# Kernel optimization log

Hardware: AMD Instinct MI355X
Metric: run time of the kernel (lower is better)

Reference implementation:

```python
import jax, jax.numpy as jnp
import numpy as np

# tcnn HashGrid config constants
N_LEVELS = 16
F_PER_LEVEL = 2
LOG2_T = 19
T = 1 << LOG2_T          # 524288 entries per level
BASE_RES = 16
PER_LEVEL_SCALE = 2.0
PRIMES = (1, 2654435761)  # tcnn spatial hash primes for 2D

N_POINTS = 4_194_304      # ~2048x2048 pixels


def setup_inputs() -> dict:
    key = jax.random.key(0)
    k1, k2, k3, k4, k5 = jax.random.split(key, 5)
    v_pixel_pos = jax.random.uniform(k1, (N_POINTS, 2), dtype=jnp.float32)
    # tcnn initializes hash grids ~ U(-1e-4, 1e-4); use scaled normals of similar magnitude
    hash_table = jax.random.normal(k2, (N_LEVELS, T, F_PER_LEVEL), dtype=jnp.float32) * 1e-4
    W1 = jax.random.normal(k3, (32, 64), dtype=jnp.float32) * (1.0 / np.sqrt(32).astype(np.float32))
    W2 = jax.random.normal(k4, (64, 64), dtype=jnp.float32) * (1.0 / np.sqrt(64).astype(np.float32))
    W3 = jax.random.normal(k5, (64, 3), dtype=jnp.float32) * (1.0 / np.sqrt(64).astype(np.float32))
    return {"v_pixel_pos": v_pixel_pos, "hash_table": hash_table, "W1": W1, "W2": W2, "W3": W3}


def _hashgrid_encode(pos, table):
    """Multiresolution hash-grid encoding, 2D bilinear. pos: [N,2] in [0,1]; table: [L,T,F]. -> [N, L*F]"""
    feats = []
    for lvl in range(N_LEVELS):  # small fixed loop over levels (structurally distinct resolutions)
        scale = BASE_RES * (PER_LEVEL_SCALE ** lvl) - 1.0
        res = int(np.ceil(scale)) + 1
        p = pos * jnp.float32(scale) + 0.5
        pf = jnp.floor(p)
        w = p - pf                       # bilinear weights, [N,2]
        pi = pf.astype(jnp.uint32)       # base corner, [N,2]
        dense = res * res <= T           # tcnn uses dense indexing when the grid fits
        acc = jnp.zeros((pos.shape[0], F_PER_LEVEL), dtype=table.dtype)
        for dx, dy in ((0, 0), (1, 0), (0, 1), (1, 1)):
            cx = pi[:, 0] + jnp.uint32(dx)
            cy = pi[:, 1] + jnp.uint32(dy)
            if dense:
                idx = cx + cy * jnp.uint32(res)
            else:
                idx = (cx * jnp.uint32(PRIMES[0])) ^ (cy * jnp.uint32(PRIMES[1]))
                idx = idx & jnp.uint32(T - 1)
            wx = w[:, 0] if dx else (1.0 - w[:, 0])
            wy = w[:, 1] if dy else (1.0 - w[:, 1])
            acc = acc + (wx * wy)[:, None] * table[lvl, idx.astype(jnp.int32)]
        feats.append(acc)
    return jnp.concatenate(feats, axis=-1)  # [N, 32]


def reference(v_pixel_pos, hash_table, W1, W2, W3):
    h = _hashgrid_encode(v_pixel_pos, hash_table)   # [N, 32]
    h = jax.nn.relu(h @ W1)                          # [N, 64]
    h = jax.nn.relu(h @ W2)                          # [N, 64]
    return h @ W3                                    # [N, 3], no output activation
```

## Files before the change

### kernel.cpp

```cpp
#include <hip/hip_runtime.h>
#include <hip/hip_fp16.h>


constexpr unsigned TSIZE  = 1u << 19;
constexpr unsigned PRIME2 = 2654435761u;
constexpr int N_HASHED    = 10;
constexpr int LVL0_HASH   = 6;
#define FEAT_SCALE   4096.0f
#define INV_SCALE    (1.0f / 4096.0f)

typedef _Float16 f16x8 __attribute__((ext_vector_type(8)));
typedef float    f32x4 __attribute__((ext_vector_type(4)));
typedef unsigned u32x2 __attribute__((ext_vector_type(2)));
typedef unsigned u32x4 __attribute__((ext_vector_type(4)));

__device__ __forceinline__ unsigned pkh2(float a, float b) {
    __half2 h = __floats2half2_rn(a, b);
    unsigned u; __builtin_memcpy(&u, &h, 4); return u;
}

__device__ __forceinline__ float2 h2f(unsigned u) {
    __half2 h; __builtin_memcpy(&h, &u, 4);
    return __half22float2(h);
}

__global__ __launch_bounds__(256)
void cvt_table(const float* __restrict__ src, unsigned* __restrict__ dst, int n2)
{
    int t = blockIdx.x * blockDim.x + threadIdx.x;
    if (t >= n2) return;
    f32x4 v = __builtin_nontemporal_load((const f32x4*)src + t);
    u32x2 pk;
    pk.x = pkh2(v.x * FEAT_SCALE, v.y * FEAT_SCALE);
    pk.y = pkh2(v.z * FEAT_SCALE, v.w * FEAT_SCALE);
    __builtin_nontemporal_store(pk, (u32x2*)dst + t);
}

__device__ __forceinline__ unsigned hash_feat(float px, float py, float scale,
                                              const unsigned* __restrict__ tblu)
{
    float pxs = fmaf(px, scale, 0.5f);
    float pys = fmaf(py, scale, 0.5f);
    float fx = floorf(pxs), fy = floorf(pys);
    float wx = pxs - fx,   wy = pys - fy;
    unsigned x0 = (unsigned)fx, y0 = (unsigned)fy;

    unsigned hy0 = y0 * PRIME2;
    unsigned hy1 = hy0 + PRIME2;
    unsigned i00 = (x0 ^ hy0) & (TSIZE - 1u);
    unsigned i01 = (x0 ^ hy1) & (TSIZE - 1u);

    unsigned u00, u10, u01, u11;
    if ((x0 & 1u) == 0u) {
        u32x2 pa = *(const u32x2*)(tblu + (i00 & ~1u));
        u32x2 pb = *(const u32x2*)(tblu + (i01 & ~1u));
        u00 = (i00 & 1u) ? pa.y : pa.x;
        u10 = (i00 & 1u) ? pa.x : pa.y;
        u01 = (i01 & 1u) ? pb.y : pb.x;
        u11 = (i01 & 1u) ? pb.x : pb.y;
    } else {
        unsigned i10 = ((x0 + 1u) ^ hy0) & (TSIZE - 1u);
        unsigned i11 = ((x0 + 1u) ^ hy1) & (TSIZE - 1u);
        u00 = tblu[i00];
        u10 = tblu[i10];
        u01 = tblu[i01];
        u11 = tblu[i11];
    }

    float2 c00 = h2f(u00), c10 = h2f(u10), c01 = h2f(u01), c11 = h2f(u11);

    float w00 = (1.0f - wx) * (1.0f - wy);
    float w10 = wx * (1.0f - wy);
    float w01 = (1.0f - wx) * wy;
    float w11 = wx * wy;

    float f0 = w00 * c00.x + w10 * c10.x + w01 * c01.x + w11 * c11.x;
    float f1 = w00 * c00.y + w10 * c10.y + w01 * c01.y + w11 * c11.y;

    return pkh2(f0, f1);
}

__global__ __launch_bounds__(256)
void encode_level(const float* __restrict__ pos,
                  const unsigned* __restrict__ tblu,
                  u32x2* __restrict__ feat,
                  int nhalf, unsigned res)
{
    int t = blockIdx.x * blockDim.x + threadIdx.x;
    if (t >= nhalf) return;
    f32x4 p = __builtin_nontemporal_load((const f32x4*)pos + t);
    float scale = (float)res - 1.0f;
    unsigned a = hash_feat(p.x, p.y, scale, tblu);
    unsigned b = hash_feat(p.z, p.w, scale, tblu);
    u32x2 pk = {a, b};
    __builtin_nontemporal_store(pk, feat + t);
}

#define S0B 80
#define S1B 144

__global__ __launch_bounds__(256)
void mlp_mfma(const float* __restrict__ pos,
              const float* __restrict__ table,
              const unsigned* __restrict__ feats,
              const float* __restrict__ W1,
              const float* __restrict__ W2,
              const float* __restrict__ W3,
              float* __restrict__ out, int n)
{
    __shared__ uint4 lds[4 * 9216 / 16];
    const int lane = threadIdx.x & 63;
    const int wid  = threadIdx.x >> 6;
    const int m    = lane & 15;
    const int q    = lane >> 4;
    char* buf = (char*)lds + wid * 9216;

    f16x8 A1[4];
#pragma unroll
    for (int ft = 0; ft < 4; ft++)
#pragma unroll
        for (int j = 0; j < 8; j++)
            A1[ft][j] = (_Float16)W1[(q * 8 + j) * 64 + ft * 16 + m];

    f16x8 A2[4][2];
#pragma unroll
    for (int ft = 0; ft < 4; ft++)
#pragma unroll
        for (int kb = 0; kb < 2; kb++)
#pragma unroll
            for (int j = 0; j < 8; j++)
                A2[ft][kb][j] = (_Float16)W2[(kb * 32 + q * 8 + j) * 64 + ft * 16 + m];

    f16x8 A3[2];
#pragma unroll
    for (int kb = 0; kb < 2; kb++)
#pragma unroll
        for (int j = 0; j < 8; j++)
            A3[kb][j] = (m < 3) ? (_Float16)W3[(kb * 32 + q * 8 + j) * 3 + m]
                                : (_Float16)0.f;

    const int ntiles  = n >> 6;
    const int wstride = gridDim.x * 4;
    const int niter   = (ntiles + wstride - 1) / wstride;

    for (int it = 0; it < niter; it++) {
        const int t = blockIdx.x * 4 + wid + it * wstride;
        const bool active = (t < ntiles);
        const int p0 = t << 6;
        const int p  = p0 + lane;

        if (active) {
            unsigned fl[16];
            float px = pos[2 * p], py = pos[2 * p + 1];
#pragma unroll
            for (int lvl = 0; lvl < 6; lvl++) {
                const unsigned res = 16u << lvl;
                const float scale = (float)res - 1.0f;
                float pxs = fmaf(px, scale, 0.5f);
                float pys = fmaf(py, scale, 0.5f);
                float fx = floorf(pxs), fy = floorf(pys);
                float wx = pxs - fx,   wy = pys - fy;
                unsigned x0 = (unsigned)fx, y0 = (unsigned)fy;
                unsigned i00 = x0 + y0 * res;
                const float* tl = table + (size_t)lvl * (size_t)TSIZE * 2u;
                float2 t00 = *(const float2*)(tl + 2u * i00);
                float2 t10 = *(const float2*)(tl + 2u * (i00 + 1u));
                float2 t01 = *(const float2*)(tl + 2u * (i00 + res));
                float2 t11 = *(const float2*)(tl + 2u * (i00 + res + 1u));
                float w00 = (1.0f - wx) * (1.0f - wy);
                float w10 = wx * (1.0f - wy);
                float w01 = (1.0f - wx) * wy;
                float w11 = wx * wy;
                float f0 = fmaf(w00, t00.x, fmaf(w10, t10.x, fmaf(w01, t01.x, w11 * t11.x)));
                float f1 = fmaf(w00, t00.y, fmaf(w10, t10.y, fmaf(w01, t01.y, w11 * t11.y)));
                fl[lvl] = pkh2(f0 * FEAT_SCALE, f1 * FEAT_SCALE);
            }
#pragma unroll
            for (int l = 0; l < N_HASHED; l++)
                fl[6 + l] = feats[(size_t)l * (size_t)n + p];

            volatile u32x4* w = (volatile u32x4*)(buf + lane * S0B);
            u32x4 w0 = {fl[0],  fl[1],  fl[2],  fl[3]};
            u32x4 w1 = {fl[4],  fl[5],  fl[6],  fl[7]};
            u32x4 w2 = {fl[8],  fl[9],  fl[10], fl[11]};
            u32x4 w3 = {fl[12], fl[13], fl[14], fl[15]};
            w[0] = w0; w[1] = w1; w[2] = w2; w[3] = w3;
        }
        __syncthreads();

        f16x8 B1[4];
        if (active) {
#pragma unroll
            for (int pt = 0; pt < 4; pt++)
                B1[pt] = *(volatile const f16x8*)(buf + (pt * 16 + m) * S0B + q * 16);
        }
        __syncthreads();

        if (active) {
#pragma unroll
            for (int ft = 0; ft < 4; ft++) {
#pragma unroll
                for (int pt = 0; pt < 4; pt++) {
                    f32x4 acc = {0.f, 0.f, 0.f, 0.f};
                    acc = __builtin_amdgcn_mfma_f32_16x16x32_f16(A1[ft], B1[pt], acc, 0, 0, 0);
                    u32x2 pk = {pkh2(fmaxf(acc[0], 0.f), fmaxf(acc[1], 0.f)),
                                pkh2(fmaxf(acc[2], 0.f), fmaxf(acc[3], 0.f))};
                    *(volatile u32x2*)(buf + (pt * 16 + m) * S1B + (ft * 16 + q * 4) * 2) = pk;
                }
            }
        }
        __syncthreads();

        f16x8 B2[4][2];
        if (active) {
#pragma unroll
            for (int pt = 0; pt < 4; pt++)
#pragma unroll
                for (int kb = 0; kb < 2; kb++)
                    B2[pt][kb] = *(volatile const f16x8*)(buf + (pt * 16 + m) * S1B + kb * 64 + q * 16);
        }
        __syncthreads();

        if (active) {
#pragma unroll
            for (int ft = 0; ft < 4; ft++) {
#pragma unroll
                for (int pt = 0; pt < 4; pt++) {
                    f32x4 acc = {0.f, 0.f, 0.f, 0.f};
                    acc = __builtin_amdgcn_mfma_f32_16x16x32_f16(A2[ft][0], B2[pt][0], acc, 0, 0, 0);
                    acc = __builtin_amdgcn_mfma_f32_16x16x32_f16(A2[ft][1], B2[pt][1], acc, 0, 0, 0);
                    u32x2 pk = {pkh2(fmaxf(acc[0], 0.f), fmaxf(acc[1], 0.f)),
                                pkh2(fmaxf(acc[2], 0.f), fmaxf(acc[3], 0.f))};
                    *(volatile u32x2*)(buf + (pt * 16 + m) * S1B + (ft * 16 + q * 4) * 2) = pk;
                }
            }
        }
        __syncthreads();

        if (active) {
            f16x8 B3[4][2];
#pragma unroll
            for (int pt = 0; pt < 4; pt++)
#pragma unroll
                for (int kb = 0; kb < 2; kb++)
                    B3[pt][kb] = *(volatile const f16x8*)(buf + (pt * 16 + m) * S1B + kb * 64 + q * 16);

#pragma unroll
            for (int pt = 0; pt < 4; pt++) {
                f32x4 acc = {0.f, 0.f, 0.f, 0.f};
                acc = __builtin_amdgcn_mfma_f32_16x16x32_f16(A3[0], B3[pt][0], acc, 0, 0, 0);
                acc = __builtin_amdgcn_mfma_f32_16x16x32_f16(A3[1], B3[pt][1], acc, 0, 0, 0);
                if (q == 0) {
                    int po = p0 + pt * 16 + m;
                    out[3 * po + 0] = acc[0] * INV_SCALE;
                    out[3 * po + 1] = acc[1] * INV_SCALE;
                    out[3 * po + 2] = acc[2] * INV_SCALE;
                }
            }
        }
        __syncthreads();
    }
}

__global__ __launch_bounds__(256, 2)
void ngp_mono(const float* __restrict__ pos, const float* __restrict__ table,
              const float* __restrict__ W1, const float* __restrict__ W2,
              const float* __restrict__ W3, float* __restrict__ out, int n)
{
    int i = blockIdx.x * blockDim.x + threadIdx.x;
    if (i >= n) return;
    float px = pos[2 * i], py = pos[2 * i + 1];
    float h1[64];
#pragma unroll
    for (int j = 0; j < 64; j++) h1[j] = 0.0f;
#pragma unroll
    for (int lvl = 0; lvl < 16; lvl++) {
        const unsigned res = 16u << lvl;
        const float scale = (float)res - 1.0f;
        float pxs = fmaf(px, scale, 0.5f);
        float pys = fmaf(py, scale, 0.5f);
        float fx = floorf(pxs), fy = floorf(pys);
        float wx = pxs - fx, wy = pys - fy;
        unsigned x0 = (unsigned)fx, y0 = (unsigned)fy;
        unsigned i00, i10, i01, i11;
        if ((unsigned long long)res * (unsigned long long)res <= (unsigned long long)TSIZE) {
            i00 = x0 + y0 * res; i10 = i00 + 1u; i01 = i00 + res; i11 = i01 + 1u;
        } else {
            unsigned hy0 = y0 * PRIME2, hy1 = (y0 + 1u) * PRIME2;
            i00 = (x0 ^ hy0) & (TSIZE - 1u);
            i10 = ((x0 + 1u) ^ hy0) & (TSIZE - 1u);
            i01 = (x0 ^ hy1) & (TSIZE - 1u);
            i11 = ((x0 + 1u) ^ hy1) & (TSIZE - 1u);
        }
        const float* tl = table + (size_t)lvl * (size_t)TSIZE * 2u;
        float2 t00 = *(const float2*)(tl + 2u * i00);
        float2 t10 = *(const float2*)(tl + 2u * i10);
        float2 t01 = *(const float2*)(tl + 2u * i01);
        float2 t11 = *(const float2*)(tl + 2u * i11);
        float w00 = (1.0f - wx) * (1.0f - wy);
        float w10 = wx * (1.0f - wy);
        float w01 = (1.0f - wx) * wy;
        float w11 = wx * wy;
        float f0 = fmaf(w00, t00.x, fmaf(w10, t10.x, fmaf(w01, t01.x, w11 * t11.x)));
        float f1 = fmaf(w00, t00.y, fmaf(w10, t10.y, fmaf(w01, t01.y, w11 * t11.y)));
        const float* w1r0 = W1 + (2 * lvl) * 64;
        const float* w1r1 = W1 + (2 * lvl + 1) * 64;
#pragma unroll
        for (int j = 0; j < 64; j++)
            h1[j] = fmaf(f0, w1r0[j], fmaf(f1, w1r1[j], h1[j]));
    }
#pragma unroll
    for (int j = 0; j < 64; j++) h1[j] = fmaxf(h1[j], 0.0f);
    float h2[64];
#pragma unroll
    for (int j = 0; j < 64; j++) h2[j] = 0.0f;
#pragma unroll
    for (int k = 0; k < 64; k++) {
        float a = h1[k];
        const float* wr = W2 + k * 64;
#pragma unroll
        for (int j = 0; j < 64; j++) h2[j] = fmaf(a, wr[j], h2[j]);
    }
#pragma unroll
    for (int j = 0; j < 64; j++) h2[j] = fmaxf(h2[j], 0.0f);
    float o0 = 0.0f, o1 = 0.0f, o2 = 0.0f;
#pragma unroll
    for (int k = 0; k < 64; k++) {
        float a = h2[k];
        o0 = fmaf(a, W3[k * 3 + 0], o0);
        o1 = fmaf(a, W3[k * 3 + 1], o1);
        o2 = fmaf(a, W3[k * 3 + 2], o2);
    }
    out[3 * i + 0] = o0; out[3 * i + 1] = o1; out[3 * i + 2] = o2;
}

extern "C" void kernel_launch(void* const* d_in, const int* in_sizes, int n_in,
                              void* d_out, int out_size, void* d_ws, size_t ws_size,
                              hipStream_t stream) {
    const float* pos   = (const float*)d_in[0];
    const float* table = (const float*)d_in[1];
    const float* W1    = (const float*)d_in[2];
    const float* W2    = (const float*)d_in[3];
    const float* W3    = (const float*)d_in[4];
    float* out = (float*)d_out;

    int n = in_sizes[0] / 2;

    size_t tbl16_bytes = (size_t)N_HASHED * TSIZE * 4u;
    size_t feats_bytes = (size_t)N_HASHED * (size_t)n * 4u;
    size_t need = tbl16_bytes + feats_bytes;

    if (ws_size < need || (n & 511)) {
        int blocks = (n + 255) / 256;
        hipLaunchKernelGGL(ngp_mono, dim3(blocks), dim3(256), 0, stream,
                           pos, table, W1, W2, W3, out, n);
        return;
    }

    unsigned* tbl16 = (unsigned*)d_ws;
    __half2* feats  = (__half2*)((char*)d_ws + tbl16_bytes);

    {
        int n2 = (N_HASHED * TSIZE) / 2;
        int blocks = (n2 + 255) / 256;
        hipLaunchKernelGGL(cvt_table, dim3(blocks), dim3(256), 0, stream,
                           table + (size_t)LVL0_HASH * TSIZE * 2u, tbl16, n2);
    }

    {
        int nhalf = n / 2;
        int blocks = (nhalf + 255) / 256;
        for (int l = 0; l < N_HASHED; l++) {
            const unsigned* tbl_l = tbl16 + (size_t)l * TSIZE;
            u32x2* feat_l = (u32x2*)(feats + (size_t)l * (size_t)n);
            unsigned res = 16u << (l + LVL0_HASH);
            hipLaunchKernelGGL(encode_level, dim3(blocks), dim3(256), 0, stream,
                               pos, tbl_l, feat_l, nhalf, res);
        }
    }

    {
        hipLaunchKernelGGL(mlp_mfma, dim3(1024), dim3(256), 0, stream,
                           pos, table, (const unsigned*)feats, W1, W2, W3, out, n);
    }
}
```

Measured before the change: 868.7 us.

## Use single-wave blocks for MLP kernel and always issue paired hash loads

The fused MLP kernel moves from 256-thread blocks of four independent waves to 64-thread single-wave blocks with a grid-stride tile loop. The active-flag guards are removed, so each __syncthreads now covers only one wave and no longer stalls waves that are at different stages. In the hash encoder, the two paired 8-byte loads are now issued unconditionally, and odd x0 adds two scalar loads on top. This removes a divergent branch at the cost of extra loads on the odd path.

```diff
diff --git a/kernel.cpp b/kernel.cpp
--- a/kernel.cpp
+++ b/kernel.cpp
@@ -50,20 +50,16 @@
     unsigned i00 = (x0 ^ hy0) & (TSIZE - 1u);
     unsigned i01 = (x0 ^ hy1) & (TSIZE - 1u);
 
-    unsigned u00, u10, u01, u11;
-    if ((x0 & 1u) == 0u) {
-        u32x2 pa = *(const u32x2*)(tblu + (i00 & ~1u));
-        u32x2 pb = *(const u32x2*)(tblu + (i01 & ~1u));
-        u00 = (i00 & 1u) ? pa.y : pa.x;
-        u10 = (i00 & 1u) ? pa.x : pa.y;
-        u01 = (i01 & 1u) ? pb.y : pb.x;
-        u11 = (i01 & 1u) ? pb.x : pb.y;
-    } else {
+    u32x2 pa = *(const u32x2*)(tblu + (i00 & ~1u));
+    u32x2 pb = *(const u32x2*)(tblu + (i01 & ~1u));
+    unsigned u00 = (i00 & 1u) ? pa.y : pa.x;
+    unsigned u01 = (i01 & 1u) ? pb.y : pb.x;
+    unsigned u10 = (i00 & 1u) ? pa.x : pa.y;
+    unsigned u11 = (i01 & 1u) ? pb.x : pb.y;
+    if (x0 & 1u) {
         unsigned i10 = ((x0 + 1u) ^ hy0) & (TSIZE - 1u);
         unsigned i11 = ((x0 + 1u) ^ hy1) & (TSIZE - 1u);
-        u00 = tblu[i00];
         u10 = tblu[i10];
-        u01 = tblu[i01];
         u11 = tblu[i11];
     }
 
@@ -99,7 +95,7 @@
 #define S0B 80
 #define S1B 144
 
-__global__ __launch_bounds__(256)
+__global__ __launch_bounds__(64)
 void mlp_mfma(const float* __restrict__ pos,
               const float* __restrict__ table,
               const unsigned* __restrict__ feats,
@@ -108,12 +104,11 @@
               const float* __restrict__ W3,
               float* __restrict__ out, int n)
 {
-    __shared__ uint4 lds[4 * 9216 / 16];
-    const int lane = threadIdx.x & 63;
-    const int wid  = threadIdx.x >> 6;
+    __shared__ uint4 lds[9216 / 16];
+    const int lane = threadIdx.x;
     const int m    = lane & 15;
     const int q    = lane >> 4;
-    char* buf = (char*)lds + wid * 9216;
+    char* buf = (char*)lds;
 
     f16x8 A1[4];
 #pragma unroll
@@ -139,17 +134,13 @@
             A3[kb][j] = (m < 3) ? (_Float16)W3[(kb * 32 + q * 8 + j) * 3 + m]
                                 : (_Float16)0.f;
 
-    const int ntiles  = n >> 6;
-    const int wstride = gridDim.x * 4;
-    const int niter   = (ntiles + wstride - 1) / wstride;
-
-    for (int it = 0; it < niter; it++) {
-        const int t = blockIdx.x * 4 + wid + it * wstride;
-        const bool active = (t < ntiles);
+    const int ntiles = n >> 6;
+
+    for (int t = blockIdx.x; t < ntiles; t += gridDim.x) {
         const int p0 = t << 6;
         const int p  = p0 + lane;
 
-        if (active) {
+        {
             unsigned fl[16];
             float px = pos[2 * p], py = pos[2 * p + 1];
 #pragma unroll
@@ -189,55 +180,47 @@
         __syncthreads();
 
         f16x8 B1[4];
-        if (active) {
-#pragma unroll
-            for (int pt = 0; pt < 4; pt++)
-                B1[pt] = *(volatile const f16x8*)(buf + (pt * 16 + m) * S0B + q * 16);
-        }
-        __syncthreads();
-
-        if (active) {
-#pragma unroll
-            for (int ft = 0; ft < 4; ft++) {
-#pragma unroll
-                for (int pt = 0; pt < 4; pt++) {
-                    f32x4 acc = {0.f, 0.f, 0.f, 0.f};
-                    acc = __builtin_amdgcn_mfma_f32_16x16x32_f16(A1[ft], B1[pt], acc, 0, 0, 0);
-                    u32x2 pk = {pkh2(fmaxf(acc[0], 0.f), fmaxf(acc[1], 0.f)),
-                                pkh2(fmaxf(acc[2], 0.f), fmaxf(acc[3], 0.f))};
-                    *(volatile u32x2*)(buf + (pt * 16 + m) * S1B + (ft * 16 + q * 4) * 2) = pk;
-                }
+#pragma unroll
+        for (int pt = 0; pt < 4; pt++)
+            B1[pt] = *(volatile const f16x8*)(buf + (pt * 16 + m) * S0B + q * 16);
+        __syncthreads();
+
+#pragma unroll
+        for (int ft = 0; ft < 4; ft++) {
+#pragma unroll
+            for (int pt = 0; pt < 4; pt++) {
+                f32x4 acc = {0.f, 0.f, 0.f, 0.f};
+                acc = __builtin_amdgcn_mfma_f32_16x16x32_f16(A1[ft], B1[pt], acc, 0, 0, 0);
+                u32x2 pk = {pkh2(fmaxf(acc[0], 0.f), fmaxf(acc[1], 0.f)),
+                            pkh2(fmaxf(acc[2], 0.f), fmaxf(acc[3], 0.f))};
+                *(volatile u32x2*)(buf + (pt * 16 + m) * S1B + (ft * 16 + q * 4) * 2) = pk;
             }
         }
         __syncthreads();
 
         f16x8 B2[4][2];
-        if (active) {
-#pragma unroll
-            for (int pt = 0; pt < 4; pt++)
-#pragma unroll
-                for (int kb = 0; kb < 2; kb++)
-                    B2[pt][kb] = *(volatile const f16x8*)(buf + (pt * 16 + m) * S1B + kb * 64 + q * 16);
-        }
-        __syncthreads();
-
-        if (active) {
-#pragma unroll
-            for (int ft = 0; ft < 4; ft++) {
-#pragma unroll
-                for (int pt = 0; pt < 4; pt++) {
-                    f32x4 acc = {0.f, 0.f, 0.f, 0.f};
-                    acc = __builtin_amdgcn_mfma_f32_16x16x32_f16(A2[ft][0], B2[pt][0], acc, 0, 0, 0);
-                    acc = __builtin_amdgcn_mfma_f32_16x16x32_f16(A2[ft][1], B2[pt][1], acc, 0, 0, 0);
-                    u32x2 pk = {pkh2(fmaxf(acc[0], 0.f), fmaxf(acc[1], 0.f)),
-                                pkh2(fmaxf(acc[2], 0.f), fmaxf(acc[3], 0.f))};
-                    *(volatile u32x2*)(buf + (pt * 16 + m) * S1B + (ft * 16 + q * 4) * 2) = pk;
-                }
+#pragma unroll
+        for (int pt = 0; pt < 4; pt++)
+#pragma unroll
+            for (int kb = 0; kb < 2; kb++)
+                B2[pt][kb] = *(volatile const f16x8*)(buf + (pt * 16 + m) * S1B + kb * 64 + q * 16);
+        __syncthreads();
+
+#pragma unroll
+        for (int ft = 0; ft < 4; ft++) {
+#pragma unroll
+            for (int pt = 0; pt < 4; pt++) {
+                f32x4 acc = {0.f, 0.f, 0.f, 0.f};
+                acc = __builtin_amdgcn_mfma_f32_16x16x32_f16(A2[ft][0], B2[pt][0], acc, 0, 0, 0);
+                acc = __builtin_amdgcn_mfma_f32_16x16x32_f16(A2[ft][1], B2[pt][1], acc, 0, 0, 0);
+                u32x2 pk = {pkh2(fmaxf(acc[0], 0.f), fmaxf(acc[1], 0.f)),
+                            pkh2(fmaxf(acc[2], 0.f), fmaxf(acc[3], 0.f))};
+                *(volatile u32x2*)(buf + (pt * 16 + m) * S1B + (ft * 16 + q * 4) * 2) = pk;
             }
         }
         __syncthreads();
 
-        if (active) {
+        {
             f16x8 B3[4][2];
 #pragma unroll
             for (int pt = 0; pt < 4; pt++)
@@ -380,7 +363,7 @@
     }
 
     {
-        hipLaunchKernelGGL(mlp_mfma, dim3(1024), dim3(256), 0, stream,
+        hipLaunchKernelGGL(mlp_mfma, dim3(4096), dim3(64), 0, stream,
                            pos, table, (const unsigned*)feats, W1, W2, W3, out, n);
     }
 }
```

After: 1.054 ms. 1.21x slower.

## Precompute dense-level features in a separate fp16 encode pass before the MLP

Applied to the files above, without the earlier changes.

Adds a new fast path that converts all 16 table levels to fp16 and computes the 6 dense levels in a dedicated encode kernel, writing their features to the workspace. A new MLP kernel then only loads 16 precomputed feature planes instead of doing dense-level gathers inline. Paired neighbour loads become one 8-byte load when x0 is even. The aim is to take the dense-level table lookups out of the MFMA kernel. In exchange the workspace grows, and an extra fp16 table conversion plus extra feature writes and reads are added.

```diff
diff --git a/kernel.cpp b/kernel.cpp
--- a/kernel.cpp
+++ b/kernel.cpp
@@ -96,8 +96,204 @@
     __builtin_nontemporal_store(pk, feat + t);
 }
 
+__device__ __forceinline__ unsigned dense_feat(float px, float py, float scale,
+                                               unsigned res,
+                                               const unsigned* __restrict__ tblu)
+{
+    float pxs = fmaf(px, scale, 0.5f);
+    float pys = fmaf(py, scale, 0.5f);
+    float fx = floorf(pxs), fy = floorf(pys);
+    float wx = pxs - fx,   wy = pys - fy;
+    unsigned x0 = (unsigned)fx, y0 = (unsigned)fy;
+    unsigned i00 = x0 + y0 * res;
+    unsigned i01 = i00 + res;
+
+    unsigned u00, u10, u01, u11;
+    if ((x0 & 1u) == 0u) {
+        u32x2 pa = *(const u32x2*)(tblu + i00);
+        u32x2 pb = *(const u32x2*)(tblu + i01);
+        u00 = pa.x; u10 = pa.y;
+        u01 = pb.x; u11 = pb.y;
+    } else {
+        u00 = tblu[i00];
+        u10 = tblu[i00 + 1u];
+        u01 = tblu[i01];
+        u11 = tblu[i01 + 1u];
+    }
+
+    float2 c00 = h2f(u00), c10 = h2f(u10), c01 = h2f(u01), c11 = h2f(u11);
+
+    float w00 = (1.0f - wx) * (1.0f - wy);
+    float w10 = wx * (1.0f - wy);
+    float w01 = (1.0f - wx) * wy;
+    float w11 = wx * wy;
+
+    float f0 = w00 * c00.x + w10 * c10.x + w01 * c01.x + w11 * c11.x;
+    float f1 = w00 * c00.y + w10 * c10.y + w01 * c01.y + w11 * c11.y;
+
+    return pkh2(f0, f1);
+}
+
+__global__ __launch_bounds__(256)
+void encode_dense(const float* __restrict__ pos,
+                  const unsigned* __restrict__ tbl16,
+                  unsigned* __restrict__ feats,
+                  int nhalf, int n)
+{
+    int t = blockIdx.x * blockDim.x + threadIdx.x;
+    if (t >= nhalf) return;
+    f32x4 p = __builtin_nontemporal_load((const f32x4*)pos + t);
+#pragma unroll
+    for (int lvl = 0; lvl < 6; lvl++) {
+        const unsigned res = 16u << lvl;
+        const float scale = (float)res - 1.0f;
+        const unsigned* tbl_l = tbl16 + (size_t)lvl * TSIZE;
+        unsigned a = dense_feat(p.x, p.y, scale, res, tbl_l);
+        unsigned b = dense_feat(p.z, p.w, scale, res, tbl_l);
+        u32x2 pk = {a, b};
+        __builtin_nontemporal_store(pk, (u32x2*)(feats + (size_t)lvl * n) + t);
+    }
+}
+
 #define S0B 80
 #define S1B 144
+
+__global__ __launch_bounds__(256)
+void mlp_mfma16(const unsigned* __restrict__ feats,
+                const float* __restrict__ W1,
+                const float* __restrict__ W2,
+                const float* __restrict__ W3,
+                float* __restrict__ out, int n)
+{
+    __shared__ uint4 lds[4 * 9216 / 16];
+    const int lane = threadIdx.x & 63;
+    const int wid  = threadIdx.x >> 6;
+    const int m    = lane & 15;
+    const int q    = lane >> 4;
+    char* buf = (char*)lds + wid * 9216;
+
+    f16x8 A1[4];
+#pragma unroll
+    for (int ft = 0; ft < 4; ft++)
+#pragma unroll
+        for (int j = 0; j < 8; j++)
+            A1[ft][j] = (_Float16)W1[(q * 8 + j) * 64 + ft * 16 + m];
+
+    f16x8 A2[4][2];
+#pragma unroll
+    for (int ft = 0; ft < 4; ft++)
+#pragma unroll
+        for (int kb = 0; kb < 2; kb++)
+#pragma unroll
+            for (int j = 0; j < 8; j++)
+                A2[ft][kb][j] = (_Float16)W2[(kb * 32 + q * 8 + j) * 64 + ft * 16 + m];
+
+    f16x8 A3[2];
+#pragma unroll
+    for (int kb = 0; kb < 2; kb++)
+#pragma unroll
+        for (int j = 0; j < 8; j++)
+            A3[kb][j] = (m < 3) ? (_Float16)W3[(kb * 32 + q * 8 + j) * 3 + m]
+                                : (_Float16)0.f;
+
+    const int ntiles  = n >> 6;
+    const int wstride = gridDim.x * 4;
+    const int niter   = (ntiles + wstride - 1) / wstride;
+
+    for (int it = 0; it < niter; it++) {
+        const int t = blockIdx.x * 4 + wid + it * wstride;
+        const bool active = (t < ntiles);
+        const int p0 = t << 6;
+        const int p  = p0 + lane;
+
+        if (active) {
+            unsigned fl[16];
+#pragma unroll
+            for (int l = 0; l < 16; l++)
+                fl[l] = __builtin_nontemporal_load(feats + (size_t)l * (size_t)n + p);
+
+            volatile u32x4* w = (volatile u32x4*)(buf + lane * S0B);
+            u32x4 w0 = {fl[0],  fl[1],  fl[2],  fl[3]};
+            u32x4 w1 = {fl[4],  fl[5],  fl[6],  fl[7]};
+            u32x4 w2 = {fl[8],  fl[9],  fl[10], fl[11]};
+            u32x4 w3 = {fl[12], fl[13], fl[14], fl[15]};
+            w[0] = w0; w[1] = w1; w[2] = w2; w[3] = w3;
+        }
+        __syncthreads();
+
+        f16x8 B1[4];
+        if (active) {
+#pragma unroll
+            for (int pt = 0; pt < 4; pt++)
+                B1[pt] = *(volatile const f16x8*)(buf + (pt * 16 + m) * S0B + q * 16);
+        }
+        __syncthreads();
+
+        if (active) {
+#pragma unroll
+            for (int ft = 0; ft < 4; ft++) {
+#pragma unroll
+                for (int pt = 0; pt < 4; pt++) {
+                    f32x4 acc = {0.f, 0.f, 0.f, 0.f};
+                    acc = __builtin_amdgcn_mfma_f32_16x16x32_f16(A1[ft], B1[pt], acc, 0, 0, 0);
+                    u32x2 pk = {pkh2(fmaxf(acc[0], 0.f), fmaxf(acc[1], 0.f)),
+                                pkh2(fmaxf(acc[2], 0.f), fmaxf(acc[3], 0.f))};
+                    *(volatile u32x2*)(buf + (pt * 16 + m) * S1B + (ft * 16 + q * 4) * 2) = pk;
+                }
+            }
+        }
+        __syncthreads();
+
+        f16x8 B2[4][2];
+        if (active) {
+#pragma unroll
+            for (int pt = 0; pt < 4; pt++)
+#pragma unroll
+                for (int kb = 0; kb < 2; kb++)
+                    B2[pt][kb] = *(volatile const f16x8*)(buf + (pt * 16 + m) * S1B + kb * 64 + q * 16);
+        }
+        __syncthreads();
+
+        if (active) {
+#pragma unroll
+            for (int ft = 0; ft < 4; ft++) {
+#pragma unroll
+                for (int pt = 0; pt < 4; pt++) {
+                    f32x4 acc = {0.f, 0.f, 0.f, 0.f};
+                    acc = __builtin_amdgcn_mfma_f32_16x16x32_f16(A2[ft][0], B2[pt][0], acc, 0, 0, 0);
+                    acc = __builtin_amdgcn_mfma_f32_16x16x32_f16(A2[ft][1], B2[pt][1], acc, 0, 0, 0);
+                    u32x2 pk = {pkh2(fmaxf(acc[0], 0.f), fmaxf(acc[1], 0.f)),
+                                pkh2(fmaxf(acc[2], 0.f), fmaxf(acc[3], 0.f))};
+                    *(volatile u32x2*)(buf + (pt * 16 + m) * S1B + (ft * 16 + q * 4) * 2) = pk;
+                }
+            }
+        }
+        __syncthreads();
+
+        if (active) {
+            f16x8 B3[4][2];
+#pragma unroll
+            for (int pt = 0; pt < 4; pt++)
+#pragma unroll
+                for (int kb = 0; kb < 2; kb++)
+                    B3[pt][kb] = *(volatile const f16x8*)(buf + (pt * 16 + m) * S1B + kb * 64 + q * 16);
+
+#pragma unroll
+            for (int pt = 0; pt < 4; pt++) {
+                f32x4 acc = {0.f, 0.f, 0.f, 0.f};
+                acc = __builtin_amdgcn_mfma_f32_16x16x32_f16(A3[0], B3[pt][0], acc, 0, 0, 0);
+                acc = __builtin_amdgcn_mfma_f32_16x16x32_f16(A3[1], B3[pt][1], acc, 0, 0, 0);
+                if (q == 0) {
+                    int po = p0 + pt * 16 + m;
+                    out[3 * po + 0] = acc[0] * INV_SCALE;
+                    out[3 * po + 1] = acc[1] * INV_SCALE;
+                    out[3 * po + 2] = acc[2] * INV_SCALE;
+                }
+            }
+        }
+        __syncthreads();
+    }
+}
 
 __global__ __launch_bounds__(256)
 void mlp_mfma(const float* __restrict__ pos,
@@ -346,41 +542,71 @@
 
     int n = in_sizes[0] / 2;
 
+    size_t tbl16_all   = 16ull * TSIZE * 4u;
+    size_t feats16_all = 16ull * (size_t)n * 4u;
+    if (ws_size >= tbl16_all + feats16_all && !(n & 511)) {
+        unsigned* tbl16 = (unsigned*)d_ws;
+        unsigned* feats = (unsigned*)((char*)d_ws + tbl16_all);
+
+        {
+            int n2 = (16 * TSIZE) / 2;
+            hipLaunchKernelGGL(cvt_table, dim3((n2 + 255) / 256), dim3(256), 0, stream,
+                               table, tbl16, n2);
+        }
+        int nhalf = n / 2;
+        {
+            hipLaunchKernelGGL(encode_dense, dim3((nhalf + 255) / 256), dim3(256), 0, stream,
+                               pos, tbl16, feats, nhalf, n);
+        }
+        {
+            int blocks = (nhalf + 255) / 256;
+            for (int l = 0; l < N_HASHED; l++) {
+                const unsigned* tbl_l = tbl16 + (size_t)(LVL0_HASH + l) * TSIZE;
+                u32x2* feat_l = (u32x2*)(feats + (size_t)(LVL0_HASH + l) * (size_t)n);
+                unsigned res = 16u << (l + LVL0_HASH);
+                hipLaunchKernelGGL(encode_level, dim3(blocks), dim3(256), 0, stream,
+                                   pos, tbl_l, feat_l, nhalf, res);
+            }
+        }
+        {
+            hipLaunchKernelGGL(mlp_mfma16, dim3(1024), dim3(256), 0, stream,
+                               feats, W1, W2, W3, out, n);
+        }
+        return;
+    }
+
     size_t tbl16_bytes = (size_t)N_HASHED * TSIZE * 4u;
     size_t feats_bytes = (size_t)N_HASHED * (size_t)n * 4u;
-    size_t need = tbl16_bytes + feats_bytes;
-
-    if (ws_size < need || (n & 511)) {
+    if (ws_size >= tbl16_bytes + feats_bytes && !(n & 511)) {
+        unsigned* tbl16 = (unsigned*)d_ws;
+        __half2* feats  = (__half2*)((char*)d_ws + tbl16_bytes);
+
+        {
+            int n2 = (N_HASHED * TSIZE) / 2;
+            hipLaunchKernelGGL(cvt_table, dim3((n2 + 255) / 256), dim3(256), 0, stream,
+                               table + (size_t)LVL0_HASH * TSIZE * 2u, tbl16, n2);
+        }
+        {
+            int nhalf = n / 2;
+            int blocks = (nhalf + 255) / 256;
+            for (int l = 0; l < N_HASHED; l++) {
+                const unsigned* tbl_l = tbl16 + (size_t)l * TSIZE;
+                u32x2* feat_l = (u32x2*)(feats + (size_t)l * (size_t)n);
+                unsigned res = 16u << (l + LVL0_HASH);
+                hipLaunchKernelGGL(encode_level, dim3(blocks), dim3(256), 0, stream,
+                                   pos, tbl_l, feat_l, nhalf, res);
+            }
+        }
+        {
+            hipLaunchKernelGGL(mlp_mfma, dim3(1024), dim3(256), 0, stream,
+                               pos, table, (const unsigned*)feats, W1, W2, W3, out, n);
+        }
+        return;
+    }
+
+    {
         int blocks = (n + 255) / 256;
         hipLaunchKernelGGL(ngp_mono, dim3(blocks), dim3(256), 0, stream,
                            pos, table, W1, W2, W3, out, n);
-        return;
-    }
-
-    unsigned* tbl16 = (unsigned*)d_ws;
-    __half2* feats  = (__half2*)((char*)d_ws + tbl16_bytes);
-
-    {
-        int n2 = (N_HASHED * TSIZE) / 2;
-        int blocks = (n2 + 255) / 256;
-        hipLaunchKernelGGL(cvt_table, dim3(blocks), dim3(256), 0, stream,
-                           table + (size_t)LVL0_HASH * TSIZE * 2u, tbl16, n2);
-    }
-
-    {
-        int nhalf = n / 2;
-        int blocks = (nhalf + 255) / 256;
-        for (int l = 0; l < N_HASHED; l++) {
-            const unsigned* tbl_l = tbl16 + (size_t)l * TSIZE;
-            u32x2* feat_l = (u32x2*)(feats + (size_t)l * (size_t)n);
-            unsigned res = 16u << (l + LVL0_HASH);
-            hipLaunchKernelGGL(encode_level, dim3(blocks), dim3(256), 0, stream,
-                               pos, tbl_l, feat_l, nhalf, res);
-        }
-    }
-
-    {
-        hipLaunchKernelGGL(mlp_mfma, dim3(1024), dim3(256), 0, stream,
-                           pos, table, (const unsigned*)feats, W1, W2, W3, out, n);
-    }
-}
+    }
+}
```

Measured after the change: 868.8 us. Within noise of the previous version (+0.0%).
